# Performance work log

Hardware: AMD Instinct MI355X
Metric: run time of the kernel (lower is better)

## Reference

```python
import jax, jax.numpy as jnp
import numpy as np

N_NODES = 100000
N_EDGES = 1200000
N_GRAPHS = 1000
NUM_SHAPES, NUM_COLORS, NUM_CLASSES = 16, 8, 10


def setup_inputs() -> dict:
    key = jax.random.key(0)
    ks = jax.random.split(key, 12)
    x = jax.random.randint(ks[0], (N_NODES, 2), 0, 8, dtype=jnp.int32)
    edge_index = jax.random.randint(ks[1], (2, N_EDGES), 0, N_NODES, dtype=jnp.int32)
    batch = jnp.sort(jax.random.randint(ks[2], (N_NODES,), 0, N_GRAPHS, dtype=jnp.int32))
    s = 0.05
    params = {
        "shape_emb": jax.random.normal(ks[3], (NUM_SHAPES, 8), jnp.float32) * s,
        "color_emb": jax.random.normal(ks[4], (NUM_COLORS, 8), jnp.float32) * s,
        "W_pre": jax.random.normal(ks[5], (32, 16), jnp.float32) * s,
        "b_pre": jnp.zeros((32,), jnp.float32),
        "W_rel1": jax.random.normal(ks[6], (64, 32), jnp.float32) * s,
        "b_rel1": jnp.zeros((64,), jnp.float32),
        "W_root1": jax.random.normal(ks[7], (64, 32), jnp.float32) * s,
        "W_rel2": jax.random.normal(ks[8], (64, 64), jnp.float32) * s,
        "b_rel2": jnp.zeros((64,), jnp.float32),
        "W_root2": jax.random.normal(ks[9], (64, 64), jnp.float32) * s,
        "W_cls": jax.random.normal(ks[10], (NUM_CLASSES, 64), jnp.float32) * s,
        "b_cls": jnp.zeros((NUM_CLASSES,), jnp.float32),
    }
    return dict(x=x, edge_index=edge_index, batch=batch, num_graphs=N_GRAPHS, **params)


def _graph_conv(h, src, dst, W_rel, b_rel, W_root, n_nodes):
    # PyG GraphConv: out = lin_rel(sum_{j in N(i)} x_j) + lin_root(x_i)
    agg = jax.ops.segment_sum(h[src], dst, num_segments=n_nodes)  # [N, d_in]
    return agg @ W_rel.T + b_rel + h @ W_root.T


def reference(x, edge_index, batch, num_graphs,
              shape_emb, color_emb, W_pre, b_pre,
              W_rel1, b_rel1, W_root1, W_rel2, b_rel2, W_root2,
              W_cls, b_cls):
    n_nodes = x.shape[0]
    src, dst = edge_index[0], edge_index[1]
    h = jnp.concatenate([shape_emb[x[:, 0]], color_emb[x[:, 1]]], axis=1)  # [N, 16]
    h = jax.nn.relu(h @ W_pre.T + b_pre)                                    # [N, 32]
    h = jax.nn.relu(_graph_conv(h, src, dst, W_rel1, b_rel1, W_root1, n_nodes))  # [N, 64]
    h = jax.nn.relu(_graph_conv(h, src, dst, W_rel2, b_rel2, W_root2, n_nodes))  # [N, 64]
    # global mean pool over graphs
    sums = jax.ops.segment_sum(h, batch, num_segments=num_graphs)           # [G, 64]
    counts = jax.ops.segment_sum(jnp.ones((n_nodes,), h.dtype), batch, num_segments=num_graphs)
    pooled = sums / jnp.maximum(counts, 1.0)[:, None]
    return pooled @ W_cls.T + b_cls                                         # [G, num_classes]
```

## Files before the change

### kernel.cpp

```cpp
#include <hip/hip_runtime.h>
#include <hip/hip_bf16.h>


#define NGRAPHS 1000
#define SCAN_CHUNK 4096
#define EPB 4096
#define SRCMASK 0x1FFFF

typedef _Float16 f16x8 __attribute__((ext_vector_type(8)));
typedef float f32x4 __attribute__((ext_vector_type(4)));

__global__ __launch_bounds__(256) void k_bcount(const int* __restrict__ dst,
                                                int* __restrict__ cnt,
                                                int nE, int nbuck)
{
    __shared__ int h[512];
    int t = threadIdx.x;
    for (int i = t; i < nbuck; i += 256) h[i] = 0;
    __syncthreads();
    int base = blockIdx.x * EPB;
#pragma unroll
    for (int q = 0; q < 16; ++q) {
        int e = base + q * 256 + t;
        if (e < nE) atomicAdd(&h[dst[e] >> 8], 1);
    }
    __syncthreads();
    int* out = cnt + (size_t)blockIdx.x * nbuck;
    for (int i = t; i < nbuck; i += 256) out[i] = h[i];
}

__global__ __launch_bounds__(256) void k_pscan_part(const int* __restrict__ cnt,
                                                    int* __restrict__ bsum,
                                                    int L, int nbuck, int nblka)
{
    __shared__ int s[256];
    int t = threadIdx.x;
    int beg = blockIdx.x * SCAN_CHUNK + t * 16;
    int sum = 0;
#pragma unroll
    for (int q = 0; q < 16; ++q) {
        int i = beg + q;
        if (i < L) {
            int b = i / nblka, k = i - b * nblka;
            sum += cnt[(size_t)k * nbuck + b];
        }
    }
    s[t] = sum;
    __syncthreads();
    for (int off = 128; off > 0; off >>= 1) {
        if (t < off) s[t] += s[t + off];
        __syncthreads();
    }
    if (t == 0) bsum[blockIdx.x] = s[0];
}

__global__ __launch_bounds__(64) void k_scan_mid(const int* __restrict__ bsum,
                                                 int* __restrict__ boffs,
                                                 int* __restrict__ row_ptr,
                                                 int B, int n)
{
    if (threadIdx.x == 0) {
        int run = 0;
        for (int b = 0; b < B; ++b) {
            boffs[b] = run;
            run += bsum[b];
        }
        row_ptr[n] = run;
    }
}

__global__ __launch_bounds__(256) void k_pscan_apply(const int* __restrict__ cnt,
                                                     const int* __restrict__ boffs,
                                                     int* __restrict__ offs_flat,
                                                     int L, int nbuck, int nblka)
{
    __shared__ int s[256];
    int t = threadIdx.x;
    int beg = blockIdx.x * SCAN_CHUNK + t * 16;
    int v[16];
    int sum = 0;
#pragma unroll
    for (int q = 0; q < 16; ++q) {
        int i = beg + q;
        if (i < L) {
            int b = i / nblka, k = i - b * nblka;
            v[q] = cnt[(size_t)k * nbuck + b];
        } else v[q] = 0;
        sum += v[q];
    }
    s[t] = sum;
    __syncthreads();
    for (int off = 1; off < 256; off <<= 1) {
        int x2 = (t >= off) ? s[t - off] : 0;
        __syncthreads();
        s[t] += x2;
        __syncthreads();
    }
    int base = boffs[blockIdx.x] + ((t == 0) ? 0 : s[t - 1]);
#pragma unroll
    for (int q = 0; q < 16; ++q) {
        int i = beg + q;
        if (i < L) {
            offs_flat[i] = base;
            base += v[q];
        }
    }
}

__global__ __launch_bounds__(256) void k_bpart(
    const int* __restrict__ src, const int* __restrict__ dst,
    const int* __restrict__ x, const int* __restrict__ offs_flat,
    unsigned* __restrict__ part, int nE, int nblka)
{
    __shared__ int h[512];
    int t = threadIdx.x;
    for (int i = t; i < 512; i += 256) h[i] = 0;
    __syncthreads();
    int base = blockIdx.x * EPB;
#pragma unroll
    for (int q = 0; q < 16; ++q) {
        int e = base + q * 256 + t;
        if (e < nE) {
            int d = dst[e];
            int b = d >> 8;
            int r = atomicAdd(&h[b], 1);
            int s = src[e];
            int2 xv = *(const int2*)(x + 2 * (size_t)s);
            unsigned code = (unsigned)((xv.x << 3) | (xv.y & 7));
            unsigned payload = ((unsigned)(d & 255) << 24) | (code << 17) | (unsigned)s;
            part[offs_flat[(size_t)b * nblka + blockIdx.x] + r] = payload;
        }
    }
}

__global__ __launch_bounds__(256) void k_bfinal(
    const unsigned* __restrict__ part, const int* __restrict__ offs_flat,
    int* __restrict__ row_ptr, int* __restrict__ sorted,
    int n, int nbuck, int nblka, int nE)
{
    __shared__ int h[256];
    __shared__ int cur[256];
    int b = blockIdx.x;
    int t = threadIdx.x;
    int ebeg = offs_flat[(size_t)b * nblka];
    int eend = (b + 1 < nbuck) ? offs_flat[(size_t)(b + 1) * nblka] : nE;

    h[t] = 0;
    __syncthreads();
    for (int e = ebeg + t; e < eend; e += 256)
        atomicAdd(&h[part[e] >> 24], 1);
    __syncthreads();
    int myv = h[t];
    for (int off = 1; off < 256; off <<= 1) {
        int x2 = (t >= off) ? h[t - off] : 0;
        __syncthreads();
        h[t] += x2;
        __syncthreads();
    }
    int excl = h[t] - myv;
    int node = b * 256 + t;
    if (node < n) row_ptr[node] = ebeg + excl;
    cur[t] = ebeg + excl;
    __syncthreads();
    for (int e = ebeg + t; e < eend; e += 256) {
        unsigned u = part[e];
        int r = atomicAdd(&cur[u >> 24], 1);
        sorted[r] = (int)(u & 0xFFFFFFu);
    }
}

__global__ __launch_bounds__(128) void k_table(
    const float* __restrict__ shape_emb, const float* __restrict__ color_emb,
    const float* __restrict__ W_pre, const float* __restrict__ b_pre,
    _Float16* __restrict__ table)
{
    int c = threadIdx.x;
    int si = c >> 3, ci = c & 7;
    float in[16];
#pragma unroll
    for (int k = 0; k < 8; ++k) in[k] = shape_emb[si * 8 + k];
#pragma unroll
    for (int k = 0; k < 8; ++k) in[8 + k] = color_emb[ci * 8 + k];
    float acc[32];
#pragma unroll
    for (int j = 0; j < 32; ++j) acc[j] = b_pre[j];
#pragma unroll
    for (int k = 0; k < 16; ++k) {
        float v = in[k];
#pragma unroll
        for (int j = 0; j < 32; ++j) acc[j] += W_pre[j * 16 + k] * v;
    }
#pragma unroll
    for (int g = 0; g < 4; ++g) {
        f16x8 o;
#pragma unroll
        for (int q = 0; q < 8; ++q) o[q] = (_Float16)fmaxf(acc[g * 8 + q], 0.f);
        *(f16x8*)(table + (size_t)c * 32 + g * 8) = o;
    }
}

__global__ __launch_bounds__(256) void k_fused1(
    const int* __restrict__ row_ptr, const int* __restrict__ sorted,
    const int* __restrict__ x, const _Float16* __restrict__ table,
    const float* __restrict__ W_rel, const float* __restrict__ b_rel,
    const float* __restrict__ W_root, _Float16* __restrict__ out, int n)
{
    __shared__ _Float16 tab[128 * 32];
    int t = threadIdx.x;
    for (int i = t * 8; i < 128 * 32; i += 2048)
        *(f16x8*)(tab + i) = *(const f16x8*)(table + i);

    int lane = t & 63;
    int w = t >> 6;
    int col = lane & 15;
    int krow = lane >> 4;

    f16x8 B[2][4];
#pragma unroll
    for (int ks = 0; ks < 2; ++ks) {
#pragma unroll
        for (int ct = 0; ct < 4; ++ct) {
            int j = ct * 16 + col;
            const float* srcw = (ks == 0 ? W_rel : W_root) + (size_t)j * 32 + krow * 8;
            float4 w0 = *(const float4*)(srcw);
            float4 w1 = *(const float4*)(srcw + 4);
            f16x8 bb;
            bb[0] = (_Float16)w0.x; bb[1] = (_Float16)w0.y;
            bb[2] = (_Float16)w0.z; bb[3] = (_Float16)w0.w;
            bb[4] = (_Float16)w1.x; bb[5] = (_Float16)w1.y;
            bb[6] = (_Float16)w1.z; bb[7] = (_Float16)w1.w;
            B[ks][ct] = bb;
        }
        __builtin_amdgcn_sched_barrier(0);
    }
    float bias[4];
#pragma unroll
    for (int ct = 0; ct < 4; ++ct) bias[ct] = b_rel[ct * 16 + col];

    __syncthreads();

    int nodebase = blockIdx.x * 128 + w * 32;
    f32x4 acc[2][4];
#pragma unroll
    for (int nt = 0; nt < 2; ++nt)
#pragma unroll
        for (int ct = 0; ct < 4; ++ct) acc[nt][ct] = (f32x4){0.f, 0.f, 0.f, 0.f};

#pragma unroll
    for (int nt = 0; nt < 2; ++nt) {
        int i = nodebase + nt * 16 + col;
        int iC = min(i, n - 1);
        int e0 = row_ptr[iC];
        int e1 = (i < n) ? row_ptr[iC + 1] : e0;

        float a[8] = {0, 0, 0, 0, 0, 0, 0, 0};
        int e = e0;
        for (; e + 2 <= e1; e += 2) {
            int c0 = sorted[e] >> 17;
            int c1 = sorted[e + 1] >> 17;
            f16x8 r0 = *(const f16x8*)(tab + c0 * 32 + krow * 8);
            f16x8 r1 = *(const f16x8*)(tab + c1 * 32 + krow * 8);
#pragma unroll
            for (int q = 0; q < 8; ++q) a[q] += (float)r0[q] + (float)r1[q];
        }
        if (e < e1) {
            int c0 = sorted[e] >> 17;
            f16x8 r0 = *(const f16x8*)(tab + c0 * 32 + krow * 8);
#pragma unroll
            for (int q = 0; q < 8; ++q) a[q] += (float)r0[q];
        }
        f16x8 Aagg;
#pragma unroll
        for (int q = 0; q < 8; ++q) Aagg[q] = (_Float16)a[q];

        int2 xv = *(const int2*)(x + 2 * (size_t)iC);
        int code = (xv.x << 3) | (xv.y & 7);
        f16x8 Aroot = *(const f16x8*)(tab + code * 32 + krow * 8);

#pragma unroll
        for (int ct = 0; ct < 4; ++ct)
            acc[nt][ct] = __builtin_amdgcn_mfma_f32_16x16x32_f16(
                Aagg, B[0][ct], acc[nt][ct], 0, 0, 0);
#pragma unroll
        for (int ct = 0; ct < 4; ++ct)
            acc[nt][ct] = __builtin_amdgcn_mfma_f32_16x16x32_f16(
                Aroot, B[1][ct], acc[nt][ct], 0, 0, 0);
    }

#pragma unroll
    for (int nt = 0; nt < 2; ++nt) {
#pragma unroll
        for (int r = 0; r < 4; ++r) {
            int node = nodebase + nt * 16 + krow * 4 + r;
            if (node < n) {
#pragma unroll
                for (int ct = 0; ct < 4; ++ct) {
                    float v = acc[nt][ct][r] + bias[ct];
                    out[(size_t)node * 64 + ct * 16 + col] = (_Float16)fmaxf(v, 0.f);
                }
            }
        }
    }
}

template <int WIDTH, int PARTS>
__global__ __launch_bounds__(256) void k_agg(
    const int* __restrict__ row_ptr, const int* __restrict__ sorted,
    const _Float16* __restrict__ h, _Float16* __restrict__ agg, int n)
{
    int tid = blockIdx.x * 256 + threadIdx.x;
    int i = tid / PARTS;
    int p = tid % PARTS;
    if (i >= n) return;
    float a[8] = {0, 0, 0, 0, 0, 0, 0, 0};
    float b[8] = {0, 0, 0, 0, 0, 0, 0, 0};
    int e0 = row_ptr[i], e1 = row_ptr[i + 1];
    const _Float16* hp = h + p * 8;
    int e = e0;
    for (; e + 4 <= e1; e += 4) {
        int s0 = sorted[e] & SRCMASK;
        int s1 = sorted[e + 1] & SRCMASK;
        int s2 = sorted[e + 2] & SRCMASK;
        int s3 = sorted[e + 3] & SRCMASK;
        f16x8 r0 = *(const f16x8*)(hp + (size_t)s0 * WIDTH);
        f16x8 r1 = *(const f16x8*)(hp + (size_t)s1 * WIDTH);
        f16x8 r2 = *(const f16x8*)(hp + (size_t)s2 * WIDTH);
        f16x8 r3 = *(const f16x8*)(hp + (size_t)s3 * WIDTH);
#pragma unroll
        for (int q = 0; q < 8; ++q) {
            a[q] += (float)r0[q] + (float)r2[q];
            b[q] += (float)r1[q] + (float)r3[q];
        }
    }
    for (; e < e1; ++e) {
        int s0 = sorted[e] & SRCMASK;
        f16x8 r0 = *(const f16x8*)(hp + (size_t)s0 * WIDTH);
#pragma unroll
        for (int q = 0; q < 8; ++q) a[q] += (float)r0[q];
    }
    f16x8 o;
#pragma unroll
    for (int q = 0; q < 8; ++q) o[q] = (_Float16)(a[q] + b[q]);
    *(f16x8*)(agg + (size_t)i * WIDTH + p * 8) = o;
}

template <int WIN>
__global__ __launch_bounds__(256) void k_conv_mfma(
    const _Float16* __restrict__ agg, const _Float16* __restrict__ h,
    const float* __restrict__ W_rel, const float* __restrict__ b_rel,
    const float* __restrict__ W_root, _Float16* __restrict__ out, int n)
{
    constexpr int NK = (2 * WIN) / 32;
    int t = threadIdx.x;
    int lane = t & 63;
    int w = t >> 6;
    int col = lane & 15;
    int krow = lane >> 4;

    f16x8 B[NK][4];
#pragma unroll
    for (int ks = 0; ks < NK; ++ks) {
#pragma unroll
        for (int ct = 0; ct < 4; ++ct) {
            int j = ct * 16 + col;
            int kb = ks * 32 + krow * 8;
            const float* srcw = (ks < NK / 2)
                ? (W_rel + (size_t)j * WIN + kb)
                : (W_root + (size_t)j * WIN + (kb - WIN));
            float4 w0 = *(const float4*)(srcw);
            float4 w1 = *(const float4*)(srcw + 4);
            f16x8 bb;
            bb[0] = (_Float16)w0.x; bb[1] = (_Float16)w0.y;
            bb[2] = (_Float16)w0.z; bb[3] = (_Float16)w0.w;
            bb[4] = (_Float16)w1.x; bb[5] = (_Float16)w1.y;
            bb[6] = (_Float16)w1.z; bb[7] = (_Float16)w1.w;
            B[ks][ct] = bb;
        }
        __builtin_amdgcn_sched_barrier(0);
    }

    float bias[4];
#pragma unroll
    for (int ct = 0; ct < 4; ++ct) bias[ct] = b_rel[ct * 16 + col];

    int nodebase = blockIdx.x * 128 + w * 32;

    f32x4 acc[2][4];
#pragma unroll
    for (int nt = 0; nt < 2; ++nt)
#pragma unroll
        for (int ct = 0; ct < 4; ++ct) acc[nt][ct] = (f32x4){0.f, 0.f, 0.f, 0.f};

#pragma unroll
    for (int ks = 0; ks < NK; ++ks) {
        const _Float16* base = (ks < NK / 2) ? agg : h;
        int koff = ((ks < NK / 2) ? ks : ks - NK / 2) * 32 + krow * 8;
#pragma unroll
        for (int nt = 0; nt < 2; ++nt) {
            int i = nodebase + nt * 16 + col;
            i = min(i, n - 1);
            f16x8 a = *(const f16x8*)(base + (size_t)i * WIN + koff);
#pragma unroll
            for (int ct = 0; ct < 4; ++ct)
                acc[nt][ct] = __builtin_amdgcn_mfma_f32_16x16x32_f16(
                    a, B[ks][ct], acc[nt][ct], 0, 0, 0);
        }
    }

#pragma unroll
    for (int nt = 0; nt < 2; ++nt) {
#pragma unroll
        for (int r = 0; r < 4; ++r) {
            int node = nodebase + nt * 16 + krow * 4 + r;
            if (node < n) {
#pragma unroll
                for (int ct = 0; ct < 4; ++ct) {
                    float v = acc[nt][ct][r] + bias[ct];
                    out[(size_t)node * 64 + ct * 16 + col] = (_Float16)fmaxf(v, 0.f);
                }
            }
        }
    }
}

__global__ __launch_bounds__(256) void k_pool_cls(
    const _Float16* __restrict__ h3, const int* __restrict__ batch,
    const float* __restrict__ W_cls, const float* __restrict__ b_cls,
    float* __restrict__ out, int n)
{
    __shared__ float part[4][64];
    __shared__ float pool[64];
    __shared__ int range[2];
    int g = blockIdx.x;
    int t = threadIdx.x;

    if (t < 2) {
        int key = g + t;
        int lo = 0, hi = n;
        while (lo < hi) {
            int mid = (lo + hi) >> 1;
            if (batch[mid] < key) lo = mid + 1; else hi = mid;
        }
        range[t] = lo;
    }
    __syncthreads();
    int start = range[0], end = range[1];

    int j = t & 63;
    int sub = t >> 6;
    float local = 0.f;
    for (int i = start + sub; i < end; i += 4)
        local += (float)h3[(size_t)i * 64 + j];
    part[sub][j] = local;
    __syncthreads();

    if (t < 64) {
        float cnt = (float)(end - start);
        float inv = 1.0f / fmaxf(cnt, 1.0f);
        pool[t] = (part[0][t] + part[1][t] + part[2][t] + part[3][t]) * inv;
    }
    __syncthreads();

    if (t < 10) {
        float acc = b_cls[t];
#pragma unroll
        for (int k = 0; k < 64; ++k) acc += W_cls[t * 64 + k] * pool[k];
        out[(size_t)g * 10 + t] = acc;
    }
}

extern "C" void kernel_launch(void* const* d_in, const int* in_sizes, int n_in,
                              void* d_out, int out_size, void* d_ws, size_t ws_size,
                              hipStream_t stream)
{
    const int* x        = (const int*)d_in[0];
    const int* ei       = (const int*)d_in[1];
    const int* batch    = (const int*)d_in[2];
    const float* shape_emb = (const float*)d_in[4];
    const float* color_emb = (const float*)d_in[5];
    const float* W_pre   = (const float*)d_in[6];
    const float* b_pre   = (const float*)d_in[7];
    const float* W_rel1  = (const float*)d_in[8];
    const float* b_rel1  = (const float*)d_in[9];
    const float* W_root1 = (const float*)d_in[10];
    const float* W_rel2  = (const float*)d_in[11];
    const float* b_rel2  = (const float*)d_in[12];
    const float* W_root2 = (const float*)d_in[13];
    const float* W_cls   = (const float*)d_in[14];
    const float* b_cls   = (const float*)d_in[15];

    const int n  = in_sizes[0] / 2;
    const int nE = in_sizes[1] / 2;
    const int G  = NGRAPHS;
    const int* src = ei;
    const int* dst = ei + nE;

    const int NBUCK = (n + 255) >> 8;
    const int NBLKA = (nE + EPB - 1) / EPB;
    const int L     = NBUCK * NBLKA;
    const int SBL   = (L + SCAN_CHUNK - 1) / SCAN_CHUNK;

    _Float16* us = (_Float16*)d_ws;
    _Float16* h2B   = us;
    _Float16* agg2B = us + (size_t)n * 64;
    _Float16* h3B   = us + (size_t)n * 128;
    _Float16* tabB  = us + (size_t)n * 192;
    int* ints      = (int*)(tabB + 128 * 32);
    int* row_ptr   = ints;
    int* cnt       = row_ptr + (n + 1);
    int* offs_flat = cnt + L;
    unsigned* part = (unsigned*)(offs_flat + L);
    int* sorted    = (int*)(part + nE);
    int* bsum      = sorted + nE;
    int* boffs     = bsum + 64;

    const int CB = (n + 127) / 128;

    k_table<<<1, 128, 0, stream>>>(shape_emb, color_emb, W_pre, b_pre, tabB);
    k_bcount<<<NBLKA, 256, 0, stream>>>(dst, cnt, nE, NBUCK);
    k_pscan_part<<<SBL, 256, 0, stream>>>(cnt, bsum, L, NBUCK, NBLKA);
    k_scan_mid<<<1, 64, 0, stream>>>(bsum, boffs, row_ptr, SBL, n);
    k_pscan_apply<<<SBL, 256, 0, stream>>>(cnt, boffs, offs_flat, L, NBUCK, NBLKA);
    k_bpart<<<NBLKA, 256, 0, stream>>>(src, dst, x, offs_flat, part, nE, NBLKA);
    k_bfinal<<<NBUCK, 256, 0, stream>>>(part, offs_flat, row_ptr, sorted,
                                        n, NBUCK, NBLKA, nE);

    k_fused1<<<CB, 256, 0, stream>>>(row_ptr, sorted, x, tabB,
                                     W_rel1, b_rel1, W_root1, h2B, n);
    k_agg<64, 8><<<((size_t)n * 8 + 255) / 256, 256, 0, stream>>>(row_ptr, sorted, h2B, agg2B, n);
    k_conv_mfma<64><<<CB, 256, 0, stream>>>(agg2B, h2B, W_rel2, b_rel2, W_root2, h3B, n);
    k_pool_cls<<<G, 256, 0, stream>>>(h3B, batch, W_cls, b_cls, (float*)d_out, n);
}
```

Baseline: 253.8 us.

## Fuse layer-2 neighbor aggregation into the MFMA conv kernel

```diff
diff --git a/kernel.cpp b/kernel.cpp
--- a/kernel.cpp
+++ b/kernel.cpp
@@ -303,70 +303,28 @@
     }
 }
 
-template <int WIDTH, int PARTS>
-__global__ __launch_bounds__(256) void k_agg(
+__global__ __launch_bounds__(256) void k_fused2(
     const int* __restrict__ row_ptr, const int* __restrict__ sorted,
-    const _Float16* __restrict__ h, _Float16* __restrict__ agg, int n)
-{
-    int tid = blockIdx.x * 256 + threadIdx.x;
-    int i = tid / PARTS;
-    int p = tid % PARTS;
-    if (i >= n) return;
-    float a[8] = {0, 0, 0, 0, 0, 0, 0, 0};
-    float b[8] = {0, 0, 0, 0, 0, 0, 0, 0};
-    int e0 = row_ptr[i], e1 = row_ptr[i + 1];
-    const _Float16* hp = h + p * 8;
-    int e = e0;
-    for (; e + 4 <= e1; e += 4) {
-        int s0 = sorted[e] & SRCMASK;
-        int s1 = sorted[e + 1] & SRCMASK;
-        int s2 = sorted[e + 2] & SRCMASK;
-        int s3 = sorted[e + 3] & SRCMASK;
-        f16x8 r0 = *(const f16x8*)(hp + (size_t)s0 * WIDTH);
-        f16x8 r1 = *(const f16x8*)(hp + (size_t)s1 * WIDTH);
-        f16x8 r2 = *(const f16x8*)(hp + (size_t)s2 * WIDTH);
-        f16x8 r3 = *(const f16x8*)(hp + (size_t)s3 * WIDTH);
-#pragma unroll
-        for (int q = 0; q < 8; ++q) {
-            a[q] += (float)r0[q] + (float)r2[q];
-            b[q] += (float)r1[q] + (float)r3[q];
-        }
-    }
-    for (; e < e1; ++e) {
-        int s0 = sorted[e] & SRCMASK;
-        f16x8 r0 = *(const f16x8*)(hp + (size_t)s0 * WIDTH);
-#pragma unroll
-        for (int q = 0; q < 8; ++q) a[q] += (float)r0[q];
-    }
-    f16x8 o;
-#pragma unroll
-    for (int q = 0; q < 8; ++q) o[q] = (_Float16)(a[q] + b[q]);
-    *(f16x8*)(agg + (size_t)i * WIDTH + p * 8) = o;
-}
-
-template <int WIN>
-__global__ __launch_bounds__(256) void k_conv_mfma(
-    const _Float16* __restrict__ agg, const _Float16* __restrict__ h,
+    const _Float16* __restrict__ h2,
     const float* __restrict__ W_rel, const float* __restrict__ b_rel,
     const float* __restrict__ W_root, _Float16* __restrict__ out, int n)
 {
-    constexpr int NK = (2 * WIN) / 32;
     int t = threadIdx.x;
     int lane = t & 63;
     int w = t >> 6;
     int col = lane & 15;
     int krow = lane >> 4;
 
-    f16x8 B[NK][4];
-#pragma unroll
-    for (int ks = 0; ks < NK; ++ks) {
+    f16x8 B[4][4];
+#pragma unroll
+    for (int ks = 0; ks < 4; ++ks) {
 #pragma unroll
         for (int ct = 0; ct < 4; ++ct) {
             int j = ct * 16 + col;
             int kb = ks * 32 + krow * 8;
-            const float* srcw = (ks < NK / 2)
-                ? (W_rel + (size_t)j * WIN + kb)
-                : (W_root + (size_t)j * WIN + (kb - WIN));
+            const float* srcw = (ks < 2)
+                ? (W_rel + (size_t)j * 64 + kb)
+                : (W_root + (size_t)j * 64 + (kb - 64));
             float4 w0 = *(const float4*)(srcw);
             float4 w1 = *(const float4*)(srcw + 4);
             f16x8 bb;
@@ -378,13 +336,11 @@
         }
         __builtin_amdgcn_sched_barrier(0);
     }
-
     float bias[4];
 #pragma unroll
     for (int ct = 0; ct < 4; ++ct) bias[ct] = b_rel[ct * 16 + col];
 
     int nodebase = blockIdx.x * 128 + w * 32;
-
     f32x4 acc[2][4];
 #pragma unroll
     for (int nt = 0; nt < 2; ++nt)
@@ -392,19 +348,65 @@
         for (int ct = 0; ct < 4; ++ct) acc[nt][ct] = (f32x4){0.f, 0.f, 0.f, 0.f};
 
 #pragma unroll
-    for (int ks = 0; ks < NK; ++ks) {
-        const _Float16* base = (ks < NK / 2) ? agg : h;
-        int koff = ((ks < NK / 2) ? ks : ks - NK / 2) * 32 + krow * 8;
-#pragma unroll
-        for (int nt = 0; nt < 2; ++nt) {
-            int i = nodebase + nt * 16 + col;
-            i = min(i, n - 1);
-            f16x8 a = *(const f16x8*)(base + (size_t)i * WIN + koff);
-#pragma unroll
-            for (int ct = 0; ct < 4; ++ct)
-                acc[nt][ct] = __builtin_amdgcn_mfma_f32_16x16x32_f16(
-                    a, B[ks][ct], acc[nt][ct], 0, 0, 0);
-        }
+    for (int nt = 0; nt < 2; ++nt) {
+        int i = nodebase + nt * 16 + col;
+        int iC = min(i, n - 1);
+        int e0 = row_ptr[iC];
+        int e1 = (i < n) ? row_ptr[iC + 1] : e0;
+
+        float a0[8] = {0, 0, 0, 0, 0, 0, 0, 0};
+        float a1[8] = {0, 0, 0, 0, 0, 0, 0, 0};
+        const _Float16* hp0 = h2 + krow * 8;
+        const _Float16* hp1 = h2 + 32 + krow * 8;
+        int e = e0;
+        for (; e + 2 <= e1; e += 2) {
+            int s0 = sorted[e] & SRCMASK;
+            int s1 = sorted[e + 1] & SRCMASK;
+            f16x8 r00 = *(const f16x8*)(hp0 + (size_t)s0 * 64);
+            f16x8 r01 = *(const f16x8*)(hp1 + (size_t)s0 * 64);
+            f16x8 r10 = *(const f16x8*)(hp0 + (size_t)s1 * 64);
+            f16x8 r11 = *(const f16x8*)(hp1 + (size_t)s1 * 64);
+#pragma unroll
+            for (int q = 0; q < 8; ++q) {
+                a0[q] += (float)r00[q] + (float)r10[q];
+                a1[q] += (float)r01[q] + (float)r11[q];
+            }
+        }
+        if (e < e1) {
+            int s0 = sorted[e] & SRCMASK;
+            f16x8 r00 = *(const f16x8*)(hp0 + (size_t)s0 * 64);
+            f16x8 r01 = *(const f16x8*)(hp1 + (size_t)s0 * 64);
+#pragma unroll
+            for (int q = 0; q < 8; ++q) {
+                a0[q] += (float)r00[q];
+                a1[q] += (float)r01[q];
+            }
+        }
+        f16x8 Aagg0, Aagg1;
+#pragma unroll
+        for (int q = 0; q < 8; ++q) {
+            Aagg0[q] = (_Float16)a0[q];
+            Aagg1[q] = (_Float16)a1[q];
+        }
+        f16x8 Aroot0 = *(const f16x8*)(h2 + (size_t)iC * 64 + krow * 8);
+        f16x8 Aroot1 = *(const f16x8*)(h2 + (size_t)iC * 64 + 32 + krow * 8);
+
+#pragma unroll
+        for (int ct = 0; ct < 4; ++ct)
+            acc[nt][ct] = __builtin_amdgcn_mfma_f32_16x16x32_f16(
+                Aagg0, B[0][ct], acc[nt][ct], 0, 0, 0);
+#pragma unroll
+        for (int ct = 0; ct < 4; ++ct)
+            acc[nt][ct] = __builtin_amdgcn_mfma_f32_16x16x32_f16(
+                Aagg1, B[1][ct], acc[nt][ct], 0, 0, 0);
+#pragma unroll
+        for (int ct = 0; ct < 4; ++ct)
+            acc[nt][ct] = __builtin_amdgcn_mfma_f32_16x16x32_f16(
+                Aroot0, B[2][ct], acc[nt][ct], 0, 0, 0);
+#pragma unroll
+        for (int ct = 0; ct < 4; ++ct)
+            acc[nt][ct] = __builtin_amdgcn_mfma_f32_16x16x32_f16(
+                Aroot1, B[3][ct], acc[nt][ct], 0, 0, 0);
     }
 
 #pragma unroll
@@ -502,9 +504,8 @@
 
     _Float16* us = (_Float16*)d_ws;
     _Float16* h2B   = us;
-    _Float16* agg2B = us + (size_t)n * 64;
-    _Float16* h3B   = us + (size_t)n * 128;
-    _Float16* tabB  = us + (size_t)n * 192;
+    _Float16* h3B   = us + (size_t)n * 64;
+    _Float16* tabB  = us + (size_t)n * 128;
     int* ints      = (int*)(tabB + 128 * 32);
     int* row_ptr   = ints;
     int* cnt       = row_ptr + (n + 1);
@@ -527,7 +528,7 @@
 
     k_fused1<<<CB, 256, 0, stream>>>(row_ptr, sorted, x, tabB,
                                      W_rel1, b_rel1, W_root1, h2B, n);
-    k_agg<64, 8><<<((size_t)n * 8 + 255) / 256, 256, 0, stream>>>(row_ptr, sorted, h2B, agg2B, n);
-    k_conv_mfma<64><<<CB, 256, 0, stream>>>(agg2B, h2B, W_rel2, b_rel2, W_root2, h3B, n);
+    k_fused2<<<CB, 256, 0, stream>>>(row_ptr, sorted, h2B,
+                                     W_rel2, b_rel2, W_root2, h3B, n);
     k_pool_cls<<<G, 256, 0, stream>>>(h3B, batch, W_cls, b_cls, (float*)d_out, n);
 }
```

After: 271.4 us. +6.9%, slower.
